# Kernel optimization log

Measured on AMD Instinct MI355X. Metric: run time of the kernel, lower is better.

The kernel has to match this reference:

```python
import jax, jax.numpy as jnp
import numpy as np

B, S, D, H = 2, 2048, 2048, 16
HD = D // H


def setup_inputs() -> dict:
    key = jax.random.key(0)
    kx, = jax.random.split(key, 1)
    return {
        "x": jax.random.normal(kx, (B, S, D), dtype=jnp.float32),
        "q_mask": jnp.ones((D, D), dtype=jnp.float32),
        "k_mask": jnp.ones((D, D), dtype=jnp.float32),
        "v_mask": jnp.ones((D, D), dtype=jnp.float32),
        "out_mask": jnp.ones((D, D), dtype=jnp.float32),
        "head_mask": jnp.ones((H,), dtype=jnp.float32),
        "attention_mask": jnp.ones((B, S), dtype=jnp.float32),
        "shared_weight": jnp.float32(1.0),
    }


def reference(x, q_mask, k_mask, v_mask, out_mask, head_mask, attention_mask, shared_weight):
    b, s, d = x.shape
    scale = jnp.float32(HD) ** -0.5

    def shared_linear(inp, mask):
        # F.linear(x, mask * shared_weight): out = inp @ (mask*sw).T
        return jnp.einsum("bsd,ed->bse", inp, mask * shared_weight)

    q = shared_linear(x, q_mask).reshape(b, s, H, HD).transpose(0, 2, 1, 3)  # [B,H,S,HD]
    k = shared_linear(x, k_mask).reshape(b, s, H, HD).transpose(0, 2, 1, 3)
    v = shared_linear(x, v_mask).reshape(b, s, H, HD).transpose(0, 2, 1, 3)

    hm = head_mask.reshape(1, H, 1, 1)
    q, k, v = q * hm, k * hm, v * hm

    scores = jnp.einsum("bhqd,bhkd->bhqk", q, k) * scale  # [B,H,S,S]

    # causal mask: upper triangle (j > i) -> -inf
    causal = jnp.triu(jnp.ones((s, s), dtype=bool), k=1)
    scores = jnp.where(causal, -jnp.inf, scores)

    # additive attention mask: (1 - m) * -10000, broadcast [B,1,1,S]
    scores = scores + (1.0 - attention_mask)[:, None, None, :] * -10000.0

    attn = jax.nn.softmax(scores, axis=-1)  # dropout is identity in eval / p=0

    out = jnp.einsum("bhqk,bhkd->bhqd", attn, v)          # [B,H,S,HD]
    out = out.transpose(0, 2, 1, 3).reshape(b, s, d)       # [B,S,D]
    return shared_linear(out, out_mask)
```

## Files before the change

kernel.cpp:

```cpp
#include <hip/hip_runtime.h>

#define B_  2
#define S_  2048
#define D_  2048
#define H_  16
#define HD_ 128

typedef __bf16 bf16;
typedef __bf16 bf16x4 __attribute__((ext_vector_type(4)));
typedef __bf16 bf16x8 __attribute__((ext_vector_type(8)));
typedef float  f32x4  __attribute__((ext_vector_type(4)));

__device__ __forceinline__ void gld_lds16(const void* g, void* l) {
    __builtin_amdgcn_global_load_lds(
        (const __attribute__((address_space(1))) unsigned int*)g,
        (__attribute__((address_space(3))) unsigned int*)l, 16, 0, 0);
}

__global__ __launch_bounds__(256)
void precast_kernel(const float* __restrict__ x, bf16* __restrict__ xh,
                    bf16* __restrict__ xl) {
    int i = (blockIdx.x * 256 + threadIdx.x) * 8;
    float4 a = *(const float4*)(x + i);
    float4 b = *(const float4*)(x + i + 4);
    float av[8] = {a.x, a.y, a.z, a.w, b.x, b.y, b.z, b.w};
    bf16x8 h8, l8;
#pragma unroll
    for (int e = 0; e < 8; e++) {
        bf16 hv = (bf16)av[e];
        h8[e] = hv;
        l8[e] = (bf16)(av[e] - (float)hv);
    }
    *(bf16x8*)(xh + i) = h8;
    *(bf16x8*)(xl + i) = l8;
}

#define BK 64

template<int MODE>
__global__ __launch_bounds__(256, 3)
void gemm_nt(const bf16* __restrict__ Ah_g, const bf16* __restrict__ Al_g,
             const float* __restrict__ B0, const float* __restrict__ B1,
             const float* __restrict__ B2,
             const float* __restrict__ swp, const float* __restrict__ hm,
             bf16* __restrict__ qh_, bf16* __restrict__ ql_,
             bf16* __restrict__ kh_, bf16* __restrict__ kl_,
             bf16* __restrict__ vp_, float* __restrict__ Cf) {
    const int K = D_;
    __shared__ bf16 Ah[128 * 64];
    __shared__ bf16 Al[128 * 64];
    __shared__ bf16 Bs[128 * 64];
    const int t = threadIdx.x;
    const int wave = t >> 6, lane = t & 63;
    const int wr = wave >> 1, wc = wave & 1;
    const int m0 = blockIdx.y * 128, n0 = blockIdx.x * 128;
    const int lrow = lane & 15, lquad = lane >> 4;
    const float sw = swp[0];

    const int which = (MODE == 0) ? (n0 >> 11) : 0;
    const bool split = (MODE == 0) && (which < 2);

    const float* Bp;
    if (MODE == 0) {
        Bp = (which == 0) ? B0 : ((which == 1) ? B1 : B2);
        Bp += (size_t)(n0 & (D_ - 1)) * K;
    } else {
        Bp = B0 + (size_t)n0 * K;
    }

    const int srow8 = lane >> 3;
    const int sgrp  = lane & 7;
    const int g0 = (lquad)     ^ (lrow & 7);
    const int g1 = (lquad + 4) ^ (lrow & 7);

    f32x4 acc[4][4];
#pragma unroll
    for (int i = 0; i < 4; i++)
#pragma unroll
        for (int j = 0; j < 4; j++) acc[i][j] = (f32x4){0.f, 0.f, 0.f, 0.f};

    for (int k0 = 0; k0 < K; k0 += BK) {
#pragma unroll
        for (int p = 0; p < 4; p++) {
            int r = wave * 32 + p * 8 + srow8;
            int gcol = (sgrp ^ (r & 7)) * 8;
            gld_lds16(Ah_g + (size_t)(m0 + r) * K + k0 + gcol,
                      &Ah[(wave * 32 + p * 8) * 64]);
            if (split)
                gld_lds16(Al_g + (size_t)(m0 + r) * K + k0 + gcol,
                          &Al[(wave * 32 + p * 8) * 64]);
        }
#pragma unroll
        for (int p = 0; p < 4; p++) {
            int r = p * 32 + (t >> 3);
            int gcol = (sgrp ^ (r & 7)) * 8;
            const float* bp = Bp + (size_t)r * K + k0 + gcol;
            float4 blo = *(const float4*)bp;
            float4 bhi = *(const float4*)(bp + 4);
            bf16x8 b8;
            b8[0] = (bf16)(blo.x * sw); b8[1] = (bf16)(blo.y * sw);
            b8[2] = (bf16)(blo.z * sw); b8[3] = (bf16)(blo.w * sw);
            b8[4] = (bf16)(bhi.x * sw); b8[5] = (bf16)(bhi.y * sw);
            b8[6] = (bf16)(bhi.z * sw); b8[7] = (bf16)(bhi.w * sw);
            *(bf16x8*)&Bs[r * 64 + sgrp * 8] = b8;
        }
        __syncthreads();

#pragma unroll
        for (int kk = 0; kk < 2; kk++) {
            const int gA = kk ? g1 : g0;
            bf16x8 afh[4], afl[4], bfr[4];
#pragma unroll
            for (int i = 0; i < 4; i++) {
                int row = wr * 64 + i * 16 + lrow;
                afh[i] = *(const bf16x8*)&Ah[row * 64 + gA * 8];
                if (split) afl[i] = *(const bf16x8*)&Al[row * 64 + gA * 8];
            }
#pragma unroll
            for (int j = 0; j < 4; j++) {
                int row = wc * 64 + j * 16 + lrow;
                bfr[j] = *(const bf16x8*)&Bs[row * 64 + gA * 8];
            }
#pragma unroll
            for (int i = 0; i < 4; i++)
#pragma unroll
                for (int j = 0; j < 4; j++) {
                    acc[i][j] = __builtin_amdgcn_mfma_f32_16x16x32_bf16(
                        afh[i], bfr[j], acc[i][j], 0, 0, 0);
                    if (split)
                        acc[i][j] = __builtin_amdgcn_mfma_f32_16x16x32_bf16(
                            afl[i], bfr[j], acc[i][j], 0, 0, 0);
                }
        }
        __syncthreads();
    }

#pragma unroll
    for (int i = 0; i < 4; i++) {
#pragma unroll
        for (int j = 0; j < 4; j++) {
#pragma unroll
            for (int r = 0; r < 4; r++) {
                int m = m0 + wr * 64 + i * 16 + lquad * 4 + r;
                int n = n0 + wc * 64 + j * 16 + lrow;
                float v = acc[i][j][r];
                if (MODE == 0) {
                    int e = n & (D_ - 1);
                    int h = e >> 7, hd = e & (HD_ - 1);
                    int b = m >> 11, s = m & (S_ - 1);
                    v *= hm[h];
                    size_t idx = (((size_t)b * H_ + h) * S_ + s) * HD_ + hd;
                    if (which == 2) {
                        vp_[idx] = (bf16)v;
                    } else {
                        bf16 hv = (bf16)v;
                        bf16 lv = (bf16)(v - (float)hv);
                        if (which == 0) { qh_[idx] = hv; ql_[idx] = lv; }
                        else            { kh_[idx] = hv; kl_[idx] = lv; }
                    }
                } else {
                    Cf[(size_t)m * D_ + n] = v;
                }
            }
        }
    }
}

#define KLD 136
#define VLD 72

__global__ __launch_bounds__(256, 2)
void attn_kernel(const bf16* __restrict__ qh_, const bf16* __restrict__ ql_,
                 const bf16* __restrict__ kh_, const bf16* __restrict__ kl_,
                 const bf16* __restrict__ v_, const float* __restrict__ am,
                 bf16* __restrict__ outp) {
    const int bh = blockIdx.x & 31;
    const int qblk = 31 - (blockIdx.x >> 5);
    const int b = bh >> 4, h = bh & 15;
    const int i0 = qblk * 64;
    const int t = threadIdx.x, wave = t >> 6, lane = t & 63;
    const int lrow = lane & 15, quad = lane >> 4;

    __shared__ bf16 skh[64 * KLD], skl[64 * KLD];
    __shared__ bf16 svt[128 * VLD];
    __shared__ bf16 sp[4][16 * VLD];

    const size_t base = (size_t)bh * S_ * HD_;

    const int qrow = i0 + wave * 16 + lrow;
    bf16x8 qhf[4], qlf[4];
#pragma unroll
    for (int c = 0; c < 4; c++) {
        qhf[c] = *(const bf16x8*)&qh_[base + (size_t)qrow * HD_ + c * 32 + quad * 8];
        qlf[c] = *(const bf16x8*)&ql_[base + (size_t)qrow * HD_ + c * 32 + quad * 8];
    }

    float m_i[4], l_i[4];
    f32x4 O[8];
#pragma unroll
    for (int r = 0; r < 4; r++) { m_i[r] = -INFINITY; l_i[r] = 0.f; }
#pragma unroll
    for (int n2 = 0; n2 < 8; n2++) O[n2] = (f32x4){0.f, 0.f, 0.f, 0.f};

    const float scale = 0.08838834764831845f;

    for (int j0 = 0; j0 <= i0; j0 += 64) {
        __syncthreads();
#pragma unroll
        for (int p = 0; p < 4; p++) {
            int idx = p * 256 + t;
            int r = idx >> 4;
            int c8 = (idx & 15) * 8;
            *(bf16x8*)&skh[r * KLD + c8] = *(const bf16x8*)&kh_[base + (size_t)(j0 + r) * HD_ + c8];
            *(bf16x8*)&skl[r * KLD + c8] = *(const bf16x8*)&kl_[base + (size_t)(j0 + r) * HD_ + c8];
        }
#pragma unroll
        for (int p = 0; p < 4; p++) {
            int d0 = (p * 4 + wave) * 8;
            bf16x8 v8 = *(const bf16x8*)&v_[base + (size_t)(j0 + lane) * HD_ + d0];
#pragma unroll
            for (int e = 0; e < 8; e++) svt[(d0 + e) * VLD + lane] = v8[e];
        }
        __syncthreads();

        float amadd[4];
#pragma unroll
        for (int nt = 0; nt < 4; nt++)
            amadd[nt] = (1.0f - am[b * S_ + j0 + nt * 16 + lrow]) * -10000.0f;

        f32x4 s4[4];
#pragma unroll
        for (int nt = 0; nt < 4; nt++) s4[nt] = (f32x4){0.f, 0.f, 0.f, 0.f};
#pragma unroll
        for (int c = 0; c < 4; c++) {
#pragma unroll
            for (int nt = 0; nt < 4; nt++) {
                bf16x8 bh8 = *(const bf16x8*)&skh[(nt * 16 + lrow) * KLD + c * 32 + quad * 8];
                bf16x8 bl8 = *(const bf16x8*)&skl[(nt * 16 + lrow) * KLD + c * 32 + quad * 8];
                s4[nt] = __builtin_amdgcn_mfma_f32_16x16x32_bf16(qhf[c], bh8, s4[nt], 0, 0, 0);
                s4[nt] = __builtin_amdgcn_mfma_f32_16x16x32_bf16(qhf[c], bl8, s4[nt], 0, 0, 0);
                s4[nt] = __builtin_amdgcn_mfma_f32_16x16x32_bf16(qlf[c], bh8, s4[nt], 0, 0, 0);
            }
        }

        const bool diag = (j0 == i0);
#pragma unroll
        for (int r = 0; r < 4; r++) {
            const int rrow = wave * 16 + quad * 4 + r;
            float sv[4], pw[4];
            float mx = -INFINITY;
#pragma unroll
            for (int nt = 0; nt < 4; nt++) {
                float xv = s4[nt][r] * scale + amadd[nt];
                if (diag && (nt * 16 + lrow) > rrow) xv = -INFINITY;
                sv[nt] = xv;
                mx = fmaxf(mx, xv);
            }
#pragma unroll
            for (int off = 1; off < 16; off <<= 1) mx = fmaxf(mx, __shfl_xor(mx, off));
            float mnew = fmaxf(m_i[r], mx);
            float alpha = __expf(m_i[r] - mnew);
            float ps = 0.f;
#pragma unroll
            for (int nt = 0; nt < 4; nt++) { pw[nt] = __expf(sv[nt] - mnew); ps += pw[nt]; }
#pragma unroll
            for (int off = 1; off < 16; off <<= 1) ps += __shfl_xor(ps, off);
            l_i[r] = l_i[r] * alpha + ps;
            m_i[r] = mnew;
#pragma unroll
            for (int n2 = 0; n2 < 8; n2++) O[n2][r] *= alpha;
#pragma unroll
            for (int nt = 0; nt < 4; nt++)
                sp[wave][(quad * 4 + r) * VLD + nt * 16 + lrow] = (bf16)pw[nt];
        }
        __asm__ volatile("s_waitcnt lgkmcnt(0)" ::: "memory");

#pragma unroll
        for (int kk2 = 0; kk2 < 64; kk2 += 32) {
            bf16x8 pf = *(const bf16x8*)&sp[wave][lrow * VLD + kk2 + quad * 8];
#pragma unroll
            for (int n2 = 0; n2 < 8; n2++) {
                bf16x8 vf8 = *(const bf16x8*)&svt[(n2 * 16 + lrow) * VLD + kk2 + quad * 8];
                O[n2] = __builtin_amdgcn_mfma_f32_16x16x32_bf16(pf, vf8, O[n2], 0, 0, 0);
            }
        }
    }

    float inv[4];
#pragma unroll
    for (int r = 0; r < 4; r++) inv[r] = 1.0f / l_i[r];
#pragma unroll
    for (int n2 = 0; n2 < 8; n2++)
#pragma unroll
        for (int r = 0; r < 4; r++) {
            int srow = i0 + wave * 16 + quad * 4 + r;
            outp[((size_t)(b * S_ + srow)) * D_ + h * HD_ + n2 * 16 + lrow] =
                (bf16)(O[n2][r] * inv[r]);
        }
}

extern "C" void kernel_launch(void* const* d_in, const int* in_sizes, int n_in,
                              void* d_out, int out_size, void* d_ws, size_t ws_size,
                              hipStream_t stream) {
    const float* x  = (const float*)d_in[0];
    const float* qm = (const float*)d_in[1];
    const float* km = (const float*)d_in[2];
    const float* vm = (const float*)d_in[3];
    const float* om = (const float*)d_in[4];
    const float* hm = (const float*)d_in[5];
    const float* am = (const float*)d_in[6];
    const float* sw = (const float*)d_in[7];
    float* out = (float*)d_out;

    const size_t P = (size_t)B_ * H_ * S_ * HD_ * sizeof(bf16);
    char* ws = (char*)d_ws;
    bf16* xh = (bf16*)(ws + 0 * P);
    bf16* xl = (bf16*)(ws + 1 * P);
    bf16* qh = (bf16*)(ws + 2 * P);
    bf16* ql = (bf16*)(ws + 3 * P);
    bf16* kh = (bf16*)(ws + 4 * P);
    bf16* kl = (bf16*)(ws + 5 * P);
    bf16* vp = (bf16*)d_out;
    bf16* attn_out = (bf16*)(ws + 0 * P);

    precast_kernel<<<(B_ * S_ * D_) / (256 * 8), 256, 0, stream>>>(x, xh, xl);

    gemm_nt<0><<<dim3(48, 32), 256, 0, stream>>>(
        xh, xl, qm, km, vm, sw, hm, qh, ql, kh, kl, vp, nullptr);

    attn_kernel<<<B_ * H_ * 32, 256, 0, stream>>>(qh, ql, kh, kl, vp, am, attn_out);

    gemm_nt<1><<<dim3(16, 32), 256, 0, stream>>>(
        attn_out, nullptr, om, nullptr, nullptr, sw, hm,
        nullptr, nullptr, nullptr, nullptr, nullptr, out);
}
```

Before: 508.7 us.

## Enlarge attention query tile and stage pre-transposed V with direct-to-LDS loads

Result: slower. 618.2 us (+21.5%).

```diff
diff --git a/kernel.cpp b/kernel.cpp
--- a/kernel.cpp
+++ b/kernel.cpp
@@ -45,7 +45,7 @@
              const float* __restrict__ swp, const float* __restrict__ hm,
              bf16* __restrict__ qh_, bf16* __restrict__ ql_,
              bf16* __restrict__ kh_, bf16* __restrict__ kl_,
-             bf16* __restrict__ vp_, float* __restrict__ Cf) {
+             bf16* __restrict__ vt_, float* __restrict__ Cf) {
     const int K = D_;
     __shared__ bf16 Ah[128 * 64];
     __shared__ bf16 Al[128 * 64];
@@ -149,10 +149,10 @@
                     int h = e >> 7, hd = e & (HD_ - 1);
                     int b = m >> 11, s = m & (S_ - 1);
                     v *= hm[h];
-                    size_t idx = (((size_t)b * H_ + h) * S_ + s) * HD_ + hd;
                     if (which == 2) {
-                        vp_[idx] = (bf16)v;
+                        vt_[((size_t)(b * H_ + h) * HD_ + hd) * S_ + s] = (bf16)v;
                     } else {
+                        size_t idx = (((size_t)b * H_ + h) * S_ + s) * HD_ + hd;
                         bf16 hv = (bf16)v;
                         bf16 lv = (bf16)(v - (float)hv);
                         if (which == 0) { qh_[idx] = hv; ql_[idx] = lv; }
@@ -166,137 +166,166 @@
     }
 }
 
-#define KLD 136
-#define VLD 72
-
 __global__ __launch_bounds__(256, 2)
 void attn_kernel(const bf16* __restrict__ qh_, const bf16* __restrict__ ql_,
                  const bf16* __restrict__ kh_, const bf16* __restrict__ kl_,
-                 const bf16* __restrict__ v_, const float* __restrict__ am,
+                 const bf16* __restrict__ vt_, const float* __restrict__ am,
                  bf16* __restrict__ outp) {
     const int bh = blockIdx.x & 31;
-    const int qblk = 31 - (blockIdx.x >> 5);
+    const int half = blockIdx.x >> 8;
+    const int qblk = half ? ((blockIdx.x - 256) >> 5) : (15 - (blockIdx.x >> 5));
     const int b = bh >> 4, h = bh & 15;
-    const int i0 = qblk * 64;
+    const int i0 = qblk * 128;
     const int t = threadIdx.x, wave = t >> 6, lane = t & 63;
     const int lrow = lane & 15, quad = lane >> 4;
 
-    __shared__ bf16 skh[64 * KLD], skl[64 * KLD];
-    __shared__ bf16 svt[128 * VLD];
-    __shared__ bf16 sp[4][16 * VLD];
-
-    const size_t base = (size_t)bh * S_ * HD_;
-
-    const int qrow = i0 + wave * 16 + lrow;
-    bf16x8 qhf[4], qlf[4];
-#pragma unroll
-    for (int c = 0; c < 4; c++) {
-        qhf[c] = *(const bf16x8*)&qh_[base + (size_t)qrow * HD_ + c * 32 + quad * 8];
-        qlf[c] = *(const bf16x8*)&ql_[base + (size_t)qrow * HD_ + c * 32 + quad * 8];
-    }
-
-    float m_i[4], l_i[4];
-    f32x4 O[8];
-#pragma unroll
-    for (int r = 0; r < 4; r++) { m_i[r] = -INFINITY; l_i[r] = 0.f; }
-#pragma unroll
-    for (int n2 = 0; n2 < 8; n2++) O[n2] = (f32x4){0.f, 0.f, 0.f, 0.f};
+    __shared__ bf16 sh[32768];
+    bf16* skh = sh;
+    bf16* skl = sh + 8192;
+    bf16* svt = sh + 16384;
+    bf16* spp = sh + 24576 + wave * 2048;
+
+    const size_t kbase = (size_t)bh * S_ * HD_;
+    const size_t vbase = (size_t)bh * HD_ * S_;
+
+    bf16x8 qhf[2][4], qlf[2][4];
+#pragma unroll
+    for (int ib = 0; ib < 2; ib++) {
+        int qrow = i0 + wave * 32 + ib * 16 + lrow;
+#pragma unroll
+        for (int c = 0; c < 4; c++) {
+            qhf[ib][c] = *(const bf16x8*)&qh_[kbase + (size_t)qrow * HD_ + c * 32 + quad * 8];
+            qlf[ib][c] = *(const bf16x8*)&ql_[kbase + (size_t)qrow * HD_ + c * 32 + quad * 8];
+        }
+    }
+
+    float m_i[2][4], l_i[2][4];
+    f32x4 O[2][8];
+#pragma unroll
+    for (int ib = 0; ib < 2; ib++) {
+#pragma unroll
+        for (int r = 0; r < 4; r++) { m_i[ib][r] = -INFINITY; l_i[ib][r] = 0.f; }
+#pragma unroll
+        for (int n2 = 0; n2 < 8; n2++) O[ib][n2] = (f32x4){0.f, 0.f, 0.f, 0.f};
+    }
 
     const float scale = 0.08838834764831845f;
-
-    for (int j0 = 0; j0 <= i0; j0 += 64) {
+    const int iwmin = i0 + wave * 32;
+    const int iwmax = iwmin + 31;
+
+    for (int j0 = 0; j0 <= i0 + 64; j0 += 64) {
         __syncthreads();
 #pragma unroll
         for (int p = 0; p < 4; p++) {
-            int idx = p * 256 + t;
-            int r = idx >> 4;
-            int c8 = (idx & 15) * 8;
-            *(bf16x8*)&skh[r * KLD + c8] = *(const bf16x8*)&kh_[base + (size_t)(j0 + r) * HD_ + c8];
-            *(bf16x8*)&skl[r * KLD + c8] = *(const bf16x8*)&kl_[base + (size_t)(j0 + r) * HD_ + c8];
+            int rb = wave * 16 + p * 4;
+            int r = rb + (lane >> 4);
+            int gl = ((lane & 15) ^ (r & 7)) * 8;
+            gld_lds16(kh_ + kbase + (size_t)(j0 + r) * HD_ + gl, &skh[rb * 128]);
+            gld_lds16(kl_ + kbase + (size_t)(j0 + r) * HD_ + gl, &skl[rb * 128]);
         }
 #pragma unroll
         for (int p = 0; p < 4; p++) {
-            int d0 = (p * 4 + wave) * 8;
-            bf16x8 v8 = *(const bf16x8*)&v_[base + (size_t)(j0 + lane) * HD_ + d0];
-#pragma unroll
-            for (int e = 0; e < 8; e++) svt[(d0 + e) * VLD + lane] = v8[e];
+            int db = wave * 32 + p * 8;
+            int d = db + (lane >> 3);
+            int gl = ((lane & 7) ^ (d & 7)) * 8;
+            gld_lds16(vt_ + vbase + (size_t)d * S_ + j0 + gl, &svt[db * 64]);
         }
         __syncthreads();
 
-        float amadd[4];
-#pragma unroll
-        for (int nt = 0; nt < 4; nt++)
-            amadd[nt] = (1.0f - am[b * S_ + j0 + nt * 16 + lrow]) * -10000.0f;
-
-        f32x4 s4[4];
-#pragma unroll
-        for (int nt = 0; nt < 4; nt++) s4[nt] = (f32x4){0.f, 0.f, 0.f, 0.f};
-#pragma unroll
-        for (int c = 0; c < 4; c++) {
-#pragma unroll
-            for (int nt = 0; nt < 4; nt++) {
-                bf16x8 bh8 = *(const bf16x8*)&skh[(nt * 16 + lrow) * KLD + c * 32 + quad * 8];
-                bf16x8 bl8 = *(const bf16x8*)&skl[(nt * 16 + lrow) * KLD + c * 32 + quad * 8];
-                s4[nt] = __builtin_amdgcn_mfma_f32_16x16x32_bf16(qhf[c], bh8, s4[nt], 0, 0, 0);
-                s4[nt] = __builtin_amdgcn_mfma_f32_16x16x32_bf16(qhf[c], bl8, s4[nt], 0, 0, 0);
-                s4[nt] = __builtin_amdgcn_mfma_f32_16x16x32_bf16(qlf[c], bh8, s4[nt], 0, 0, 0);
-            }
-        }
-
-        const bool diag = (j0 == i0);
-#pragma unroll
-        for (int r = 0; r < 4; r++) {
-            const int rrow = wave * 16 + quad * 4 + r;
-            float sv[4], pw[4];
-            float mx = -INFINITY;
-#pragma unroll
-            for (int nt = 0; nt < 4; nt++) {
-                float xv = s4[nt][r] * scale + amadd[nt];
-                if (diag && (nt * 16 + lrow) > rrow) xv = -INFINITY;
-                sv[nt] = xv;
-                mx = fmaxf(mx, xv);
-            }
-#pragma unroll
-            for (int off = 1; off < 16; off <<= 1) mx = fmaxf(mx, __shfl_xor(mx, off));
-            float mnew = fmaxf(m_i[r], mx);
-            float alpha = __expf(m_i[r] - mnew);
-            float ps = 0.f;
-#pragma unroll
-            for (int nt = 0; nt < 4; nt++) { pw[nt] = __expf(sv[nt] - mnew); ps += pw[nt]; }
-#pragma unroll
-            for (int off = 1; off < 16; off <<= 1) ps += __shfl_xor(ps, off);
-            l_i[r] = l_i[r] * alpha + ps;
-            m_i[r] = mnew;
-#pragma unroll
-            for (int n2 = 0; n2 < 8; n2++) O[n2][r] *= alpha;
+        if (j0 <= iwmax) {
+            float amadd[4];
 #pragma unroll
             for (int nt = 0; nt < 4; nt++)
-                sp[wave][(quad * 4 + r) * VLD + nt * 16 + lrow] = (bf16)pw[nt];
-        }
-        __asm__ volatile("s_waitcnt lgkmcnt(0)" ::: "memory");
-
-#pragma unroll
-        for (int kk2 = 0; kk2 < 64; kk2 += 32) {
-            bf16x8 pf = *(const bf16x8*)&sp[wave][lrow * VLD + kk2 + quad * 8];
-#pragma unroll
-            for (int n2 = 0; n2 < 8; n2++) {
-                bf16x8 vf8 = *(const bf16x8*)&svt[(n2 * 16 + lrow) * VLD + kk2 + quad * 8];
-                O[n2] = __builtin_amdgcn_mfma_f32_16x16x32_bf16(pf, vf8, O[n2], 0, 0, 0);
-            }
-        }
-    }
-
-    float inv[4];
-#pragma unroll
-    for (int r = 0; r < 4; r++) inv[r] = 1.0f / l_i[r];
-#pragma unroll
-    for (int n2 = 0; n2 < 8; n2++)
-#pragma unroll
-        for (int r = 0; r < 4; r++) {
-            int srow = i0 + wave * 16 + quad * 4 + r;
-            outp[((size_t)(b * S_ + srow)) * D_ + h * HD_ + n2 * 16 + lrow] =
-                (bf16)(O[n2][r] * inv[r]);
-        }
+                amadd[nt] = (1.0f - am[b * S_ + j0 + nt * 16 + lrow]) * -10000.0f;
+
+            f32x4 s4[2][4];
+#pragma unroll
+            for (int ib = 0; ib < 2; ib++)
+#pragma unroll
+                for (int nt = 0; nt < 4; nt++) s4[ib][nt] = (f32x4){0.f, 0.f, 0.f, 0.f};
+#pragma unroll
+            for (int c = 0; c < 4; c++) {
+#pragma unroll
+                for (int nt = 0; nt < 4; nt++) {
+                    int ka = (nt * 16 + lrow) * 128 + (((c * 4 + quad) ^ (lrow & 7)) * 8);
+                    bf16x8 kb8 = *(const bf16x8*)&skh[ka];
+                    bf16x8 lb8 = *(const bf16x8*)&skl[ka];
+#pragma unroll
+                    for (int ib = 0; ib < 2; ib++) {
+                        s4[ib][nt] = __builtin_amdgcn_mfma_f32_16x16x32_bf16(qhf[ib][c], kb8, s4[ib][nt], 0, 0, 0);
+                        s4[ib][nt] = __builtin_amdgcn_mfma_f32_16x16x32_bf16(qhf[ib][c], lb8, s4[ib][nt], 0, 0, 0);
+                        s4[ib][nt] = __builtin_amdgcn_mfma_f32_16x16x32_bf16(qlf[ib][c], kb8, s4[ib][nt], 0, 0, 0);
+                    }
+                }
+            }
+
+            const bool msk = (j0 + 63 >= iwmin);
+#pragma unroll
+            for (int ib = 0; ib < 2; ib++) {
+#pragma unroll
+                for (int r = 0; r < 4; r++) {
+                    const int irow = iwmin + ib * 16 + quad * 4 + r;
+                    float sv[4], pw[4];
+                    float mx = -INFINITY;
+#pragma unroll
+                    for (int nt = 0; nt < 4; nt++) {
+                        float xv = s4[ib][nt][r] * scale + amadd[nt];
+                        if (msk && (j0 + nt * 16 + lrow) > irow) xv = -INFINITY;
+                        sv[nt] = xv;
+                        mx = fmaxf(mx, xv);
+                    }
+#pragma unroll
+                    for (int off = 1; off < 16; off <<= 1) mx = fmaxf(mx, __shfl_xor(mx, off));
+                    float mnew = fmaxf(m_i[ib][r], mx);
+                    float alpha = __expf(m_i[ib][r] - mnew);
+                    float ps = 0.f;
+#pragma unroll
+                    for (int nt = 0; nt < 4; nt++) { pw[nt] = __expf(sv[nt] - mnew); ps += pw[nt]; }
+#pragma unroll
+                    for (int off = 1; off < 16; off <<= 1) ps += __shfl_xor(ps, off);
+                    l_i[ib][r] = l_i[ib][r] * alpha + ps;
+                    m_i[ib][r] = mnew;
+#pragma unroll
+                    for (int n2 = 0; n2 < 8; n2++) O[ib][n2][r] *= alpha;
+                    const int rl = ib * 16 + quad * 4 + r;
+#pragma unroll
+                    for (int nt = 0; nt < 4; nt++) {
+                        int phys = (nt * 2 + (lrow >> 3)) ^ (rl & 7);
+                        spp[rl * 64 + phys * 8 + (lrow & 7)] = (bf16)pw[nt];
+                    }
+                }
+            }
+            __asm__ volatile("s_waitcnt lgkmcnt(0)" ::: "memory");
+
+#pragma unroll
+            for (int k2 = 0; k2 < 2; k2++) {
+                const int gp = ((quad + k2 * 4) ^ (lrow & 7)) * 8;
+                bf16x8 pf0 = *(const bf16x8*)&spp[(lrow) * 64 + gp];
+                bf16x8 pf1 = *(const bf16x8*)&spp[(16 + lrow) * 64 + gp];
+#pragma unroll
+                for (int n2 = 0; n2 < 8; n2++) {
+                    bf16x8 vf8 = *(const bf16x8*)&svt[(n2 * 16 + lrow) * 64 + gp];
+                    O[0][n2] = __builtin_amdgcn_mfma_f32_16x16x32_bf16(pf0, vf8, O[0][n2], 0, 0, 0);
+                    O[1][n2] = __builtin_amdgcn_mfma_f32_16x16x32_bf16(pf1, vf8, O[1][n2], 0, 0, 0);
+                }
+            }
+        }
+    }
+
+#pragma unroll
+    for (int ib = 0; ib < 2; ib++) {
+        float inv[4];
+#pragma unroll
+        for (int r = 0; r < 4; r++) inv[r] = 1.0f / l_i[ib][r];
+#pragma unroll
+        for (int n2 = 0; n2 < 8; n2++)
+#pragma unroll
+            for (int r = 0; r < 4; r++) {
+                int srow = iwmin + ib * 16 + quad * 4 + r;
+                outp[((size_t)(b * S_ + srow)) * D_ + h * HD_ + n2 * 16 + lrow] =
+                    (bf16)(O[ib][n2][r] * inv[r]);
+            }
+    }
 }
 
 extern "C" void kernel_launch(void* const* d_in, const int* in_sizes, int n_in,
@@ -320,15 +349,15 @@
     bf16* ql = (bf16*)(ws + 3 * P);
     bf16* kh = (bf16*)(ws + 4 * P);
     bf16* kl = (bf16*)(ws + 5 * P);
-    bf16* vp = (bf16*)d_out;
+    bf16* vt = (bf16*)d_out;
     bf16* attn_out = (bf16*)(ws + 0 * P);
 
     precast_kernel<<<(B_ * S_ * D_) / (256 * 8), 256, 0, stream>>>(x, xh, xl);
 
     gemm_nt<0><<<dim3(48, 32), 256, 0, stream>>>(
-        xh, xl, qm, km, vm, sw, hm, qh, ql, kh, kl, vp, nullptr);
-
-    attn_kernel<<<B_ * H_ * 32, 256, 0, stream>>>(qh, ql, kh, kl, vp, am, attn_out);
+        xh, xl, qm, km, vm, sw, hm, qh, ql, kh, kl, vt, nullptr);
+
+    attn_kernel<<<512, 256, 0, stream>>>(qh, ql, kh, kl, vt, am, attn_out);
 
     gemm_nt<1><<<dim3(16, 32), 256, 0, stream>>>(
         attn_out, nullptr, om, nullptr, nullptr, sw, hm,
```

## Pre-transpose V and stream K/V tiles into LDS with direct global-to-LDS loads

Applied to the files above, without the earlier changes.

New measurement: 493.7 us. -3.0%, faster.

```diff
diff --git a/kernel.cpp b/kernel.cpp
--- a/kernel.cpp
+++ b/kernel.cpp
@@ -33,6 +33,38 @@
     }
     *(bf16x8*)(xh + i) = h8;
     *(bf16x8*)(xl + i) = l8;
+}
+
+__global__ __launch_bounds__(256)
+void transpose_v(const bf16* __restrict__ vp, bf16* __restrict__ vt) {
+    const int bh = blockIdx.x >> 5;
+    const int s0 = (blockIdx.x & 31) * 64;
+    const int t = threadIdx.x;
+    __shared__ bf16 tile[128 * 72];
+    const bf16* src = vp + (size_t)bh * S_ * HD_;
+    bf16* dst = vt + (size_t)bh * HD_ * S_;
+
+    {
+        int r = t >> 2;
+        int g = (t & 3) * 4;
+#pragma unroll
+        for (int w = 0; w < 4; w++) {
+            bf16x8 v8 = *(const bf16x8*)&src[(size_t)(s0 + r) * HD_ + (g + w) * 8];
+#pragma unroll
+            for (int e = 0; e < 8; e++) tile[((g + w) * 8 + e) * 72 + r] = v8[e];
+        }
+    }
+    __syncthreads();
+    {
+        int d = t >> 1;
+        int sg0 = (t & 1) * 4;
+#pragma unroll
+        for (int w = 0; w < 4; w++) {
+            int sg = sg0 + w;
+            *(bf16x8*)&dst[(size_t)d * S_ + s0 + sg * 8] =
+                *(const bf16x8*)&tile[d * 72 + sg * 8];
+        }
+    }
 }
 
 #define BK 64
@@ -166,13 +198,12 @@
     }
 }
 
-#define KLD 136
-#define VLD 72
+#define SPLD 72
 
 __global__ __launch_bounds__(256, 2)
 void attn_kernel(const bf16* __restrict__ qh_, const bf16* __restrict__ ql_,
                  const bf16* __restrict__ kh_, const bf16* __restrict__ kl_,
-                 const bf16* __restrict__ v_, const float* __restrict__ am,
+                 const bf16* __restrict__ vt_, const float* __restrict__ am,
                  bf16* __restrict__ outp) {
     const int bh = blockIdx.x & 31;
     const int qblk = 31 - (blockIdx.x >> 5);
@@ -181,18 +212,20 @@
     const int t = threadIdx.x, wave = t >> 6, lane = t & 63;
     const int lrow = lane & 15, quad = lane >> 4;
 
-    __shared__ bf16 skh[64 * KLD], skl[64 * KLD];
-    __shared__ bf16 svt[128 * VLD];
-    __shared__ bf16 sp[4][16 * VLD];
-
-    const size_t base = (size_t)bh * S_ * HD_;
+    __shared__ bf16 skh[64 * 128];
+    __shared__ bf16 skl[64 * 128];
+    __shared__ bf16 svt[128 * 64];
+    __shared__ bf16 sp[4][16 * SPLD];
+
+    const size_t kbase = (size_t)bh * S_ * HD_;
+    const size_t vbase = (size_t)bh * HD_ * S_;
 
     const int qrow = i0 + wave * 16 + lrow;
     bf16x8 qhf[4], qlf[4];
 #pragma unroll
     for (int c = 0; c < 4; c++) {
-        qhf[c] = *(const bf16x8*)&qh_[base + (size_t)qrow * HD_ + c * 32 + quad * 8];
-        qlf[c] = *(const bf16x8*)&ql_[base + (size_t)qrow * HD_ + c * 32 + quad * 8];
+        qhf[c] = *(const bf16x8*)&qh_[kbase + (size_t)qrow * HD_ + c * 32 + quad * 8];
+        qlf[c] = *(const bf16x8*)&ql_[kbase + (size_t)qrow * HD_ + c * 32 + quad * 8];
     }
 
     float m_i[4], l_i[4];
@@ -208,18 +241,18 @@
         __syncthreads();
 #pragma unroll
         for (int p = 0; p < 4; p++) {
-            int idx = p * 256 + t;
-            int r = idx >> 4;
-            int c8 = (idx & 15) * 8;
-            *(bf16x8*)&skh[r * KLD + c8] = *(const bf16x8*)&kh_[base + (size_t)(j0 + r) * HD_ + c8];
-            *(bf16x8*)&skl[r * KLD + c8] = *(const bf16x8*)&kl_[base + (size_t)(j0 + r) * HD_ + c8];
+            int rb = wave * 16 + p * 4;
+            int r = rb + (lane >> 4);
+            int gl = ((lane & 15) ^ (r & 7)) * 8;
+            gld_lds16(kh_ + kbase + (size_t)(j0 + r) * HD_ + gl, &skh[rb * 128]);
+            gld_lds16(kl_ + kbase + (size_t)(j0 + r) * HD_ + gl, &skl[rb * 128]);
         }
 #pragma unroll
         for (int p = 0; p < 4; p++) {
-            int d0 = (p * 4 + wave) * 8;
-            bf16x8 v8 = *(const bf16x8*)&v_[base + (size_t)(j0 + lane) * HD_ + d0];
-#pragma unroll
-            for (int e = 0; e < 8; e++) svt[(d0 + e) * VLD + lane] = v8[e];
+            int db = wave * 32 + p * 8;
+            int d = db + (lane >> 3);
+            int gl = ((lane & 7) ^ (d & 7)) * 8;
+            gld_lds16(vt_ + vbase + (size_t)d * S_ + j0 + gl, &svt[db * 64]);
         }
         __syncthreads();
 
@@ -235,11 +268,12 @@
         for (int c = 0; c < 4; c++) {
 #pragma unroll
             for (int nt = 0; nt < 4; nt++) {
-                bf16x8 bh8 = *(const bf16x8*)&skh[(nt * 16 + lrow) * KLD + c * 32 + quad * 8];
-                bf16x8 bl8 = *(const bf16x8*)&skl[(nt * 16 + lrow) * KLD + c * 32 + quad * 8];
-                s4[nt] = __builtin_amdgcn_mfma_f32_16x16x32_bf16(qhf[c], bh8, s4[nt], 0, 0, 0);
-                s4[nt] = __builtin_amdgcn_mfma_f32_16x16x32_bf16(qhf[c], bl8, s4[nt], 0, 0, 0);
-                s4[nt] = __builtin_amdgcn_mfma_f32_16x16x32_bf16(qlf[c], bh8, s4[nt], 0, 0, 0);
+                int ka = (nt * 16 + lrow) * 128 + (((c * 4 + quad) ^ (lrow & 7)) * 8);
+                bf16x8 kb8 = *(const bf16x8*)&skh[ka];
+                bf16x8 lb8 = *(const bf16x8*)&skl[ka];
+                s4[nt] = __builtin_amdgcn_mfma_f32_16x16x32_bf16(qhf[c], kb8, s4[nt], 0, 0, 0);
+                s4[nt] = __builtin_amdgcn_mfma_f32_16x16x32_bf16(qhf[c], lb8, s4[nt], 0, 0, 0);
+                s4[nt] = __builtin_amdgcn_mfma_f32_16x16x32_bf16(qlf[c], kb8, s4[nt], 0, 0, 0);
             }
         }
 
@@ -271,16 +305,17 @@
             for (int n2 = 0; n2 < 8; n2++) O[n2][r] *= alpha;
 #pragma unroll
             for (int nt = 0; nt < 4; nt++)
-                sp[wave][(quad * 4 + r) * VLD + nt * 16 + lrow] = (bf16)pw[nt];
+                sp[wave][(quad * 4 + r) * SPLD + nt * 16 + lrow] = (bf16)pw[nt];
         }
         __asm__ volatile("s_waitcnt lgkmcnt(0)" ::: "memory");
 
 #pragma unroll
-        for (int kk2 = 0; kk2 < 64; kk2 += 32) {
-            bf16x8 pf = *(const bf16x8*)&sp[wave][lrow * VLD + kk2 + quad * 8];
+        for (int k2 = 0; k2 < 2; k2++) {
+            bf16x8 pf = *(const bf16x8*)&sp[wave][lrow * SPLD + k2 * 32 + quad * 8];
+            const int gp = ((quad + k2 * 4) ^ (lrow & 7)) * 8;
 #pragma unroll
             for (int n2 = 0; n2 < 8; n2++) {
-                bf16x8 vf8 = *(const bf16x8*)&svt[(n2 * 16 + lrow) * VLD + kk2 + quad * 8];
+                bf16x8 vf8 = *(const bf16x8*)&svt[(n2 * 16 + lrow) * 64 + gp];
                 O[n2] = __builtin_amdgcn_mfma_f32_16x16x32_bf16(pf, vf8, O[n2], 0, 0, 0);
             }
         }
@@ -321,6 +356,7 @@
     bf16* kh = (bf16*)(ws + 4 * P);
     bf16* kl = (bf16*)(ws + 5 * P);
     bf16* vp = (bf16*)d_out;
+    bf16* vt = (bf16*)((char*)d_out + P);
     bf16* attn_out = (bf16*)(ws + 0 * P);
 
     precast_kernel<<<(B_ * S_ * D_) / (256 * 8), 256, 0, stream>>>(x, xh, xl);
@@ -328,7 +364,9 @@
     gemm_nt<0><<<dim3(48, 32), 256, 0, stream>>>(
         xh, xl, qm, km, vm, sw, hm, qh, ql, kh, kl, vp, nullptr);
 
-    attn_kernel<<<B_ * H_ * 32, 256, 0, stream>>>(qh, ql, kh, kl, vp, am, attn_out);
+    transpose_v<<<1024, 256, 0, stream>>>(vp, vt);
+
+    attn_kernel<<<1024, 256, 0, stream>>>(qh, ql, kh, kl, vt, am, attn_out);
 
     gemm_nt<1><<<dim3(16, 32), 256, 0, stream>>>(
         attn_out, nullptr, om, nullptr, nullptr, sw, hm,
```
